# Performance work log

Measured on AMD Instinct MI355X. Metric: run time of the kernel, lower is better.

Reference implementation:

```python
import jax, jax.numpy as jnp
import numpy as np
import math

B, S, HID = 2, 2048, 2048
NH, HD = 16, HID // 16          # num_heads, head_dim
RING = 4
CH = S // RING                  # chunk size per ring rank
SEG_LEN = 2048                  # segment_lengths[0]
DIL = 2                         # dilation_rates[0]


def setup_inputs() -> dict:
    key = jax.random.key(0)
    k1, k2, k3 = jax.random.split(key, 3)
    x = jax.random.normal(k1, (B, S, HID), dtype=jnp.float32)
    # Linear weights stored input-major so y = x @ W (same math as torch x @ W.T)
    W_qkv = jax.random.normal(k2, (HID, 3 * HID), dtype=jnp.float32) * 0.02
    W_out = jax.random.normal(k3, (HID, HID), dtype=jnp.float32) * 0.02
    return {"x": x, "W_qkv": W_qkv, "W_out": W_out}


def _dilated_mask():
    # mask[i, j] = (segment(i) == segment(j)) and (|i - j| % DIL == 0)
    pos = jnp.arange(S)
    seg = pos // SEG_LEN
    same_seg = seg[:, None] == seg[None, :]
    dil_ok = (jnp.abs(pos[:, None] - pos[None, :]) % DIL) == 0
    return same_seg & dil_ok  # [S, S] bool


def reference(x, W_qkv, W_out):
    qkv = (x @ W_qkv).reshape(B, S, 3, NH, HD)
    q, k, v = jnp.moveaxis(qkv, 2, 0)          # each [B, S, NH, HD]
    q = jnp.transpose(q, (0, 2, 1, 3))          # [B, NH, S, HD]
    k = jnp.transpose(k, (0, 2, 1, 3))
    v = jnp.transpose(v, (0, 2, 1, 3))

    scores = jnp.einsum('bhqd,bhkd->bhqk', q, k) / math.sqrt(HD)  # [B,NH,S,S]
    if DIL > 1:
        scores = jnp.where(_dilated_mask()[None, None], scores, -jnp.inf)

    # Reshape into (q-chunk, kv-chunk) blocks to reproduce the per-chunk
    # (non-rescaled) softmax of the ring loop: each kv chunk subtracts its OWN
    # max, exps, and the un-rescaled numerators/denominators are summed.
    s = scores.reshape(B, NH, RING, CH, RING, CH)        # [B,H,Rq,Cq,Rk,Ck]
    m = jnp.max(s, axis=-1, keepdims=True)               # per-kv-chunk row max
    e = jnp.exp(s - m)                                   # -inf -> 0
    v_ch = v.reshape(B, NH, RING, CH, HD)                # [B,H,Rk,Ck,HD]
    num = jnp.einsum('bhqcrk,bhrkd->bhqcd', e, v_ch)     # [B,H,Rq,Cq,HD]
    den = jnp.sum(e, axis=(-2, -1))[..., None]           # [B,H,Rq,Cq,1]
    out = num / (den + 1e-8)

    out = out.reshape(B, NH, S, HD)
    out = jnp.transpose(out, (0, 2, 1, 3)).reshape(B, S, HID)
    return out @ W_out
```

## Files before the change

### kernel.cpp

```cpp
#include <hip/hip_runtime.h>
#include <stdint.h>

typedef float  f32x4  __attribute__((ext_vector_type(4)));
typedef __bf16 bf16x8 __attribute__((ext_vector_type(8)));

#define AS1 __attribute__((address_space(1)))
#define AS3 __attribute__((address_space(3)))


__global__ void k_cvt_all(const float* __restrict__ x, __bf16* __restrict__ xb,
                          const float* __restrict__ wqkv, __bf16* __restrict__ wqkvb,
                          const float* __restrict__ wout, __bf16* __restrict__ woutb) {
  __shared__ float tile[64][65];
  const int bx = blockIdx.x, t = threadIdx.x;
  if (bx < 4096) {
    const int d = bx * 256 + t;
    const int row = d & 127, kg = (d >> 7) & 3, mbkt = d >> 9;
    const int mb = mbkt & 31, kt = mbkt >> 5;
    const int m = mb * 128 + row, k0 = kt * 32 + kg * 8;
    const float4 v0 = *reinterpret_cast<const float4*>(x + (size_t)m * 2048 + k0);
    const float4 v1 = *reinterpret_cast<const float4*>(x + (size_t)m * 2048 + k0 + 4);
    bf16x8 o;
    o[0] = (__bf16)v0.x; o[1] = (__bf16)v0.y; o[2] = (__bf16)v0.z; o[3] = (__bf16)v0.w;
    o[4] = (__bf16)v1.x; o[5] = (__bf16)v1.y; o[6] = (__bf16)v1.z; o[7] = (__bf16)v1.w;
    *reinterpret_cast<bf16x8*>(xb + (size_t)d * 8) = o;
    return;
  }
  const float* w; __bf16* wt; int N, NBK, i0;
  if (bx < 7168) { w = wqkv; wt = wqkvb; N = 6144; NBK = 48; i0 = bx - 4096; }
  else           { w = wout; wt = woutb; N = 2048; NBK = 16; i0 = bx - 7168; }
  const int k0 = (i0 & 31) * 64, n0 = (i0 >> 5) * 64;
  #pragma unroll
  for (int i = 0; i < 16; ++i) {
    const int idx = t + 256 * i;
    const int r = idx >> 6, c = idx & 63;
    tile[r][c] = w[(size_t)(k0 + r) * N + n0 + c];
  }
  __syncthreads();
  #pragma unroll
  for (int i = 0; i < 2; ++i) {
    const int v = t + 256 * i;
    const int kb = v >> 6, nn = v & 63;
    const int n = n0 + nn, k = k0 + kb * 8;
    bf16x8 o;
    #pragma unroll
    for (int j = 0; j < 8; ++j) o[j] = (__bf16)tile[kb * 8 + j][nn];
    const size_t dst = ((size_t)(k >> 5) * NBK + (n >> 7)) * 4096 +
                       (size_t)((k >> 3) & 3) * 1024 + (n & 127) * 8;
    *reinterpret_cast<bf16x8*>(wt + dst) = o;
  }
}

template<int NBB, int CHK, int EPI>
__global__ __launch_bounds__(256, 3) void k_gemm_r8(
    const __bf16* __restrict__ Ab, const __bf16* __restrict__ Bb,
    __bf16* __restrict__ Oq, __bf16* __restrict__ Ok, __bf16* __restrict__ Ov,
    float* __restrict__ Of) {
  __shared__ __bf16 SU[6][4096];
  const int tid = threadIdx.x;
  const int w = tid >> 6, l = tid & 63, g = l >> 4, l15 = l & 15;
  const int wr = w >> 1, wc = w & 1;
  const int bx = blockIdx.x;
  const int wid = (bx & 7) * CHK + (bx >> 3);
  const int nb = wid % NBB, mb = wid / NBB;
  const size_t Abase = (size_t)mb * 4096, Bbase = (size_t)nb * 4096;
  const size_t Astep = (size_t)32 * 4096, Bstep = (size_t)NBB * 4096;
  const int soff = w * 1024;

  f32x4 acc[4][4] = {};

  auto STAGE = [&](int t, int b) {
    const __bf16* as_ = Ab + (size_t)t * Astep + Abase + soff + l * 8;
    const __bf16* bs_ = Bb + (size_t)t * Bstep + Bbase + soff + l * 8;
    __builtin_amdgcn_global_load_lds((const AS1 uint32_t*)as_,
                                     (AS3 uint32_t*)(&SU[b][soff]), 16, 0, 0);
    __builtin_amdgcn_global_load_lds((const AS1 uint32_t*)(as_ + 512),
                                     (AS3 uint32_t*)(&SU[b][soff + 512]), 16, 0, 0);
    __builtin_amdgcn_global_load_lds((const AS1 uint32_t*)bs_,
                                     (AS3 uint32_t*)(&SU[3 + b][soff]), 16, 0, 0);
    __builtin_amdgcn_global_load_lds((const AS1 uint32_t*)(bs_ + 512),
                                     (AS3 uint32_t*)(&SU[3 + b][soff + 512]), 16, 0, 0);
  };

  STAGE(0, 0);
  STAGE(1, 1);
  asm volatile("s_waitcnt vmcnt(4)" ::: "memory");
  __builtin_amdgcn_s_barrier();

  int cur = 0;
  for (int t = 0; t < 64; ++t) {
    int b2 = cur + 2; if (b2 >= 3) b2 -= 3;
    if (t + 2 < 64) STAGE(t + 2, b2);
    const __bf16* Ar = &SU[cur][g * 1024 + (wr * 64 + l15) * 8];
    const __bf16* Br = &SU[3 + cur][g * 1024 + (wc * 64 + l15) * 8];
    bf16x8 af[4], bfr[4];
    #pragma unroll
    for (int mi = 0; mi < 4; ++mi) af[mi] = *reinterpret_cast<const bf16x8*>(Ar + mi * 128);
    #pragma unroll
    for (int ni = 0; ni < 4; ++ni) bfr[ni] = *reinterpret_cast<const bf16x8*>(Br + ni * 128);
    __builtin_amdgcn_s_setprio(1);
    #pragma unroll
    for (int mi = 0; mi < 4; ++mi)
      #pragma unroll
      for (int ni = 0; ni < 4; ++ni)
        acc[mi][ni] = __builtin_amdgcn_mfma_f32_16x16x32_bf16(af[mi], bfr[ni], acc[mi][ni], 0, 0, 0);
    __builtin_amdgcn_s_setprio(0);
    __builtin_amdgcn_sched_barrier(0);
    if (t < 62) asm volatile("s_waitcnt vmcnt(4)" ::: "memory");
    else        asm volatile("s_waitcnt vmcnt(0)" ::: "memory");
    __builtin_amdgcn_s_barrier();
    cur = cur + 1; if (cur >= 3) cur -= 3;
  }

  if constexpr (EPI == 1) {
    const int m0 = mb * 128, n0 = nb * 128;
    const int ty = n0 >> 11;
    const int h = (n0 & 2047) >> 7;
    if (ty != 2) {
      #pragma unroll
      for (int mi = 0; mi < 4; ++mi) {
        #pragma unroll
        for (int r = 0; r < 4; ++r) {
          const int m = m0 + wr * 64 + mi * 16 + 4 * g + r;
          const int s = m & 2047;
          const int sp = s & 1, s2 = s >> 1;
          const int bb = m >> 11;
          const size_t base = ((((size_t)bb * 16 + h) * 2 + sp) << 17);
          #pragma unroll
          for (int ni = 0; ni < 4; ++ni) {
            const int d = wc * 64 + ni * 16 + l15;
            const __bf16 v = (__bf16)acc[mi][ni][r];
            if (ty == 0) Oq[base + (size_t)s2 * 128 + d] = v;
            else         Ok[base + (size_t)s2 * 128 + d] = v;
          }
        }
      }
    } else {
      __bf16* T = &SU[0][0];
      #pragma unroll
      for (int mi = 0; mi < 4; ++mi)
        #pragma unroll
        for (int r = 0; r < 4; ++r)
          #pragma unroll
          for (int ni = 0; ni < 4; ++ni)
            T[(size_t)(wr * 64 + mi * 16 + 4 * g + r) * 136 + wc * 64 + ni * 16 + l15] =
                (__bf16)acc[mi][ni][r];
      __syncthreads();
      const int d = tid >> 1, sp = tid & 1;
      const int bb = m0 >> 11;
      const size_t vbase = ((((size_t)bb * 16 + h) * 2 + sp) << 17) +
                           (size_t)d * 1024 + ((m0 & 2047) >> 1);
      #pragma unroll
      for (int j = 0; j < 8; ++j) {
        bf16x8 o;
        #pragma unroll
        for (int q = 0; q < 8; ++q)
          o[q] = T[(size_t)(16 * j + 2 * q + sp) * 136 + d];
        *reinterpret_cast<bf16x8*>(Ov + vbase + 8 * j) = o;
      }
    }
  } else {
    #pragma unroll
    for (int mi = 0; mi < 4; ++mi)
      #pragma unroll
      for (int r = 0; r < 4; ++r) {
        const int m = mb * 128 + wr * 64 + mi * 16 + 4 * g + r;
        #pragma unroll
        for (int ni = 0; ni < 4; ++ni) {
          const int n = nb * 128 + wc * 64 + ni * 16 + l15;
          Of[(size_t)m * 2048 + n] = acc[mi][ni][r];
        }
      }
  }
}

__global__ __launch_bounds__(256, 2) void k_attn(
    const __bf16* __restrict__ Qp, const __bf16* __restrict__ Kp,
    const __bf16* __restrict__ Vt, __bf16* __restrict__ attnA) {
  __shared__ __bf16 U[3][8192];
  __shared__ __bf16 E[4][16][136];

  const int bx = blockIdx.x;
  const int wid = (bx & 7) * 128 + (bx >> 3);
  const int qt = wid & 15, pp = (wid >> 4) & 1, h = (wid >> 5) & 15, b = wid >> 9;
  const int tid = threadIdx.x;
  const int w = tid >> 6, l = tid & 63, g = l >> 4, l15 = l & 15;
  const size_t base = ((((size_t)b * 16 + h) * 2 + pp) << 17);
  const __bf16* Qb = Qp + base;
  const __bf16* Kb = Kp + base;
  const __bf16* Vb = Vt + base;
  const int q0 = qt * 64 + w * 16;
  const float SC = 1.4426950408889634f / 11.313708498984761f;

  const int krow_in = l >> 4;
  const int vrow_in = l >> 3;
  const int vsrc_e = (((l & 7) * 16) ^ (vrow_in << 4)) >> 1;

  bf16x8 qf[4];
  #pragma unroll
  for (int ks = 0; ks < 4; ++ks)
    qf[ks] = *reinterpret_cast<const bf16x8*>(Qb + (size_t)(q0 + l15) * 128 + ks * 32 + 8 * g);

  f32x4 num[8] = {};
  float den[4] = {0.f, 0.f, 0.f, 0.f};
  f32x4 s[16];

  auto STAGE = [&](int p) {
    const int c = p >> 3, j = p & 7, bi = p % 3;
    if (j < 4) {
      #pragma unroll
      for (int i = 0; i < 4; ++i) {
        const int ch = w * 4 + i;
        const int row = ch * 4 + krow_in;
        const int cb = (l15 * 16) ^ ((row & 7) << 4);
        const __bf16* src = Kb + (size_t)(c * 256 + j * 64 + row) * 128 + (cb >> 1);
        __builtin_amdgcn_global_load_lds((const AS1 uint32_t*)src,
                                         (AS3 uint32_t*)(&U[bi][ch * 512]), 16, 0, 0);
      }
    } else {
      const int kv0 = c * 256 + ((j - 4) >> 1) * 128 + ((j - 4) & 1) * 64;
      #pragma unroll
      for (int i = 0; i < 4; ++i) {
        const int ch = w * 4 + i;
        const int row = ch * 8 + vrow_in;
        const __bf16* src = Vb + (size_t)row * 1024 + kv0 + vsrc_e;
        __builtin_amdgcn_global_load_lds((const AS1 uint32_t*)src,
                                         (AS3 uint32_t*)(&U[bi][ch * 512]), 16, 0, 0);
      }
    }
  };
  auto ENDPHASE = [&](int p) {
    if (p <= 29)      asm volatile("s_waitcnt vmcnt(4)" ::: "memory");
    else if (p == 30) asm volatile("s_waitcnt vmcnt(0)" ::: "memory");
    if (p < 31) __builtin_amdgcn_s_barrier();
  };

  STAGE(0);
  STAGE(1);
  asm volatile("s_waitcnt vmcnt(4)" ::: "memory");
  __builtin_amdgcn_s_barrier();

  for (int c = 0; c < 4; ++c) {
    const int pb = 8 * c;
    #pragma unroll
    for (int i = 0; i < 16; ++i) s[i] = f32x4{0.f, 0.f, 0.f, 0.f};
    #pragma unroll
    for (int st = 0; st < 4; ++st) {
      const int p = pb + st;
      if (p + 2 < 32) STAGE(p + 2);
      const __bf16* Kbuf = U[p % 3];
      __builtin_amdgcn_s_setprio(1);
      #pragma unroll
      for (int ks = 0; ks < 4; ++ks) {
        #pragma unroll
        for (int nf2 = 0; nf2 < 4; ++nf2) {
          const int r = nf2 * 16 + l15;
          const int cb = (ks * 64 + g * 16) ^ ((r & 7) << 4);
          const bf16x8 kf = *reinterpret_cast<const bf16x8*>(Kbuf + r * 128 + (cb >> 1));
          s[st * 4 + nf2] = __builtin_amdgcn_mfma_f32_16x16x32_bf16(qf[ks], kf, s[st * 4 + nf2], 0, 0, 0);
        }
      }
      __builtin_amdgcn_s_setprio(0);
      __builtin_amdgcn_sched_barrier(0);
      ENDPHASE(p);
    }
    float mv[4];
    #pragma unroll
    for (int r = 0; r < 4; ++r) {
      float m0v = s[0][r];
      #pragma unroll
      for (int nf = 1; nf < 16; ++nf) m0v = fmaxf(m0v, s[nf][r]);
      m0v = fmaxf(m0v, __shfl_xor(m0v, 1));
      m0v = fmaxf(m0v, __shfl_xor(m0v, 2));
      m0v = fmaxf(m0v, __shfl_xor(m0v, 4));
      m0v = fmaxf(m0v, __shfl_xor(m0v, 8));
      mv[r] = m0v;
    }
    #pragma unroll
    for (int r = 0; r < 4; ++r) {
      float ds = 0.f;
      #pragma unroll
      for (int nf = 0; nf < 16; ++nf) {
        const float e = exp2f((s[nf][r] - mv[r]) * SC);
        s[nf][r] = e;
        ds += e;
      }
      den[r] += ds;
    }
    #pragma unroll
    for (int h2 = 0; h2 < 2; ++h2) {
      #pragma unroll
      for (int nf = 0; nf < 8; ++nf)
        #pragma unroll
        for (int r = 0; r < 4; ++r)
          E[w][4 * g + r][nf * 16 + l15] = (__bf16)s[h2 * 8 + nf][r];
      #pragma unroll
      for (int sv = 0; sv < 2; ++sv) {
        const int p = pb + 4 + h2 * 2 + sv;
        if (p + 2 < 32) STAGE(p + 2);
        const __bf16* Vbuf = U[p % 3];
        __builtin_amdgcn_s_setprio(1);
        #pragma unroll
        for (int ks2 = 0; ks2 < 2; ++ks2) {
          const bf16x8 a = *reinterpret_cast<const bf16x8*>(
              &E[w][l15][sv * 64 + ks2 * 32 + 8 * g]);
          #pragma unroll
          for (int nd = 0; nd < 8; ++nd) {
            const int d = nd * 16 + l15;
            const int cb = (ks2 * 64 + g * 16) ^ ((d & 7) << 4);
            const bf16x8 vf = *reinterpret_cast<const bf16x8*>(Vbuf + d * 64 + (cb >> 1));
            num[nd] = __builtin_amdgcn_mfma_f32_16x16x32_bf16(a, vf, num[nd], 0, 0, 0);
          }
        }
        __builtin_amdgcn_s_setprio(0);
        __builtin_amdgcn_sched_barrier(0);
        ENDPHASE(p);
      }
    }
  }

  #pragma unroll
  for (int r = 0; r < 4; ++r) {
    den[r] += __shfl_xor(den[r], 1);
    den[r] += __shfl_xor(den[r], 2);
    den[r] += __shfl_xor(den[r], 4);
    den[r] += __shfl_xor(den[r], 8);
    den[r] += 1e-8f;
  }

  #pragma unroll
  for (int nd = 0; nd < 8; ++nd)
    #pragma unroll
    for (int r = 0; r < 4; ++r) {
      const int sq = q0 + 4 * g + r;
      const int srow = 2 * sq + pp;
      const int m = b * 2048 + srow;
      const int k = h * 128 + nd * 16 + l15;
      const size_t dst = ((size_t)(k >> 5) * 32 + (m >> 7)) * 4096 +
                         (size_t)((k >> 3) & 3) * 1024 + (m & 127) * 8 + (k & 7);
      attnA[dst] = (__bf16)(num[nd][r] / den[r]);
    }
}

extern "C" void kernel_launch(void* const* d_in, const int* in_sizes, int n_in,
                              void* d_out, int out_size, void* d_ws, size_t ws_size,
                              hipStream_t stream) {
  (void)in_sizes; (void)n_in; (void)out_size; (void)ws_size;
  const float* x    = (const float*)d_in[0];
  const float* wqkv = (const float*)d_in[1];
  const float* wout = (const float*)d_in[2];
  float* out = (float*)d_out;
  uint8_t* ws = (uint8_t*)d_ws;

  __bf16* xbf   = (__bf16*)(ws + 0);
  __bf16* wqkvt = (__bf16*)(ws + (16ull << 20));
  __bf16* woutt = (__bf16*)(ws + (40ull << 20));
  __bf16* Qp    = (__bf16*)(ws + (48ull << 20));
  __bf16* Kp    = (__bf16*)(ws + (64ull << 20));
  __bf16* Vt    = (__bf16*)(ws + (80ull << 20));
  __bf16* attnA = (__bf16*)(ws + 0);

  k_cvt_all<<<8192, 256, 0, stream>>>(x, xbf, wqkv, wqkvt, wout, woutt);
  k_gemm_r8<48, 192, 1><<<1536, 256, 0, stream>>>(xbf, wqkvt, Qp, Kp, Vt, nullptr);
  k_attn<<<1024, 256, 0, stream>>>(Qp, Kp, Vt, attnA);
  k_gemm_r8<16, 64, 2><<<512, 256, 0, stream>>>(attnA, woutt, nullptr, nullptr, nullptr, out);
}
```

Measured before the change: 249.6 us.

## Load GEMM B fragments directly into registers and remap blocks to per-XCD N-strips

The B operand now skips the LDS staging path. It is loaded straight from global memory into registers one k-step ahead, double-buffered via a 2x unrolled loop, while A keeps the triple-buffered global_load_lds pipeline. The block-to-tile mapping changes so each XCD owns a fixed strip of N-blocks and walks M, aiming for better L2 reuse of B per XCD. This cuts LDS traffic and barrier pressure for B but adds VGPRs for two B fragment sets, and the per-lane global reads are less coalesced.

```diff
diff --git a/kernel.cpp b/kernel.cpp
--- a/kernel.cpp
+++ b/kernel.cpp
@@ -51,8 +51,8 @@
   }
 }
 
-template<int NBB, int CHK, int EPI>
-__global__ __launch_bounds__(256, 3) void k_gemm_r8(
+template<int NBB, int STRIP, int EPI>
+__global__ __launch_bounds__(256, 3) void k_gemm_v10(
     const __bf16* __restrict__ Ab, const __bf16* __restrict__ Bb,
     __bf16* __restrict__ Oq, __bf16* __restrict__ Ok, __bf16* __restrict__ Ov,
     float* __restrict__ Of) {
@@ -61,54 +61,64 @@
   const int w = tid >> 6, l = tid & 63, g = l >> 4, l15 = l & 15;
   const int wr = w >> 1, wc = w & 1;
   const int bx = blockIdx.x;
-  const int wid = (bx & 7) * CHK + (bx >> 3);
-  const int nb = wid % NBB, mb = wid / NBB;
+  const int xcd = bx & 7, win = bx >> 3;
+  const int nb = xcd * STRIP + win % STRIP;
+  const int mb = win / STRIP;
   const size_t Abase = (size_t)mb * 4096, Bbase = (size_t)nb * 4096;
   const size_t Astep = (size_t)32 * 4096, Bstep = (size_t)NBB * 4096;
   const int soff = w * 1024;
+  const int bfo = g * 1024 + (wc * 64 + l15) * 8;
 
   f32x4 acc[4][4] = {};
 
-  auto STAGE = [&](int t, int b) {
+  auto STAGE_A = [&](int t, int b) {
     const __bf16* as_ = Ab + (size_t)t * Astep + Abase + soff + l * 8;
-    const __bf16* bs_ = Bb + (size_t)t * Bstep + Bbase + soff + l * 8;
     __builtin_amdgcn_global_load_lds((const AS1 uint32_t*)as_,
                                      (AS3 uint32_t*)(&SU[b][soff]), 16, 0, 0);
     __builtin_amdgcn_global_load_lds((const AS1 uint32_t*)(as_ + 512),
                                      (AS3 uint32_t*)(&SU[b][soff + 512]), 16, 0, 0);
-    __builtin_amdgcn_global_load_lds((const AS1 uint32_t*)bs_,
-                                     (AS3 uint32_t*)(&SU[3 + b][soff]), 16, 0, 0);
-    __builtin_amdgcn_global_load_lds((const AS1 uint32_t*)(bs_ + 512),
-                                     (AS3 uint32_t*)(&SU[3 + b][soff + 512]), 16, 0, 0);
-  };
-
-  STAGE(0, 0);
-  STAGE(1, 1);
-  asm volatile("s_waitcnt vmcnt(4)" ::: "memory");
+  };
+  auto LOADB = [&](bf16x8 (&fb)[4], int t) {
+    const __bf16* bp = Bb + (size_t)t * Bstep + Bbase + bfo;
+    #pragma unroll
+    for (int ni = 0; ni < 4; ++ni)
+      fb[ni] = *reinterpret_cast<const bf16x8*>(bp + ni * 128);
+  };
+
+  bf16x8 bA[4], bB[4];
+
+  STAGE_A(0, 0);
+  STAGE_A(1, 1);
+  LOADB(bA, 0);
+  asm volatile("s_waitcnt vmcnt(6)" ::: "memory");
   __builtin_amdgcn_s_barrier();
 
-  int cur = 0;
-  for (int t = 0; t < 64; ++t) {
+  auto body = [&](int t, int cur, bf16x8 (&bcur)[4], bf16x8 (&bnxt)[4]) {
     int b2 = cur + 2; if (b2 >= 3) b2 -= 3;
-    if (t + 2 < 64) STAGE(t + 2, b2);
+    if (t + 2 < 64) STAGE_A(t + 2, b2);
+    if (t + 1 < 64) LOADB(bnxt, t + 1);
     const __bf16* Ar = &SU[cur][g * 1024 + (wr * 64 + l15) * 8];
-    const __bf16* Br = &SU[3 + cur][g * 1024 + (wc * 64 + l15) * 8];
-    bf16x8 af[4], bfr[4];
+    bf16x8 af[4];
     #pragma unroll
     for (int mi = 0; mi < 4; ++mi) af[mi] = *reinterpret_cast<const bf16x8*>(Ar + mi * 128);
-    #pragma unroll
-    for (int ni = 0; ni < 4; ++ni) bfr[ni] = *reinterpret_cast<const bf16x8*>(Br + ni * 128);
     __builtin_amdgcn_s_setprio(1);
     #pragma unroll
     for (int mi = 0; mi < 4; ++mi)
       #pragma unroll
       for (int ni = 0; ni < 4; ++ni)
-        acc[mi][ni] = __builtin_amdgcn_mfma_f32_16x16x32_bf16(af[mi], bfr[ni], acc[mi][ni], 0, 0, 0);
+        acc[mi][ni] = __builtin_amdgcn_mfma_f32_16x16x32_bf16(af[mi], bcur[ni], acc[mi][ni], 0, 0, 0);
     __builtin_amdgcn_s_setprio(0);
     __builtin_amdgcn_sched_barrier(0);
-    if (t < 62) asm volatile("s_waitcnt vmcnt(4)" ::: "memory");
+    if (t < 62) asm volatile("s_waitcnt vmcnt(6)" ::: "memory");
     else        asm volatile("s_waitcnt vmcnt(0)" ::: "memory");
     __builtin_amdgcn_s_barrier();
+  };
+
+  int cur = 0;
+  for (int tt = 0; tt < 32; ++tt) {
+    body(2 * tt, cur, bA, bB);
+    cur = cur + 1; if (cur >= 3) cur -= 3;
+    body(2 * tt + 1, cur, bB, bA);
     cur = cur + 1; if (cur >= 3) cur -= 3;
   }
 
@@ -361,7 +371,7 @@
   __bf16* attnA = (__bf16*)(ws + 0);
 
   k_cvt_all<<<8192, 256, 0, stream>>>(x, xbf, wqkv, wqkvt, wout, woutt);
-  k_gemm_r8<48, 192, 1><<<1536, 256, 0, stream>>>(xbf, wqkvt, Qp, Kp, Vt, nullptr);
+  k_gemm_v10<48, 6, 1><<<1536, 256, 0, stream>>>(xbf, wqkvt, Qp, Kp, Vt, nullptr);
   k_attn<<<1024, 256, 0, stream>>>(Qp, Kp, Vt, attnA);
-  k_gemm_r8<16, 64, 2><<<512, 256, 0, stream>>>(attnA, woutt, nullptr, nullptr, nullptr, out);
+  k_gemm_v10<16, 2, 2><<<512, 256, 0, stream>>>(attnA, woutt, nullptr, nullptr, nullptr, out);
 }
```

New measurement: 249.4 us. No clear change (-0.1%).
